# Optimization experiments

Measured on AMD Instinct MI355X. Metric: run time of the kernel, lower is better.

Reference implementation:

```python
import jax, jax.numpy as jnp
import numpy as np

PAD = 0
SOS = 1
NEG = -1e9


def _lstm_scan(x, Wih, Whh, b, h0, c0, reverse=False):
    # x: [T, B, in]; torch gate order i, f, g, o
    def step(carry, xt):
        h, c = carry
        g = xt @ Wih.T + h @ Whh.T + b
        i, f, gg, o = jnp.split(g, 4, axis=-1)
        c = jax.nn.sigmoid(f) * c + jax.nn.sigmoid(i) * jnp.tanh(gg)
        h = jax.nn.sigmoid(o) * jnp.tanh(c)
        return (h, c), h
    (hT, cT), hs = jax.lax.scan(step, (h0, c0), x, reverse=reverse)
    return hs, hT, cT


def setup_inputs() -> dict:
    B, Ts, Tt = 32, 64, 66
    E, H, V = 512, 512, 16000
    key = jax.random.key(0)
    ks = jax.random.split(key, 16)
    s = 0.05
    n = lambda k, shape: (jax.random.normal(k, shape, dtype=jnp.float32) * s)
    return {
        'src_sentences': jax.random.randint(ks[0], (B, Ts), 4, V),
        'trg_sentences': jax.random.randint(ks[1], (B, Tt), 4, V),
        'src_emb': n(ks[2], (V, E)),
        'trg_emb': n(ks[3], (V, E)),
        'enc0_Wih': n(ks[4], (2, 4 * H, E)),
        'enc0_Whh': n(ks[5], (2, 4 * H, H)),
        'enc0_b': n(ks[6], (2, 4 * H)),
        'enc1_Wih': n(ks[7], (2, 4 * H, 2 * H)),
        'enc1_Whh': n(ks[8], (2, 4 * H, H)),
        'enc1_b': n(ks[9], (2, 4 * H)),
        'dec_Wih': n(ks[10], (8 * H, E)),      # LSTMCell: hidden = 2H -> 4*(2H) gates
        'dec_Whh': n(ks[11], (8 * H, 2 * H)),
        'dec_b': n(ks[12], (8 * H)),
        'out_W1': n(ks[13], (H, 4 * H)),
        'out_W2': n(ks[14], (V - 4, H)),
    }


def reference(src_sentences, trg_sentences, src_emb, trg_emb,
              enc0_Wih, enc0_Whh, enc0_b, enc1_Wih, enc1_Whh, enc1_b,
              dec_Wih, dec_Whh, dec_b, out_W1, out_W2):
    B, Ts = src_sentences.shape
    Tt = trg_sentences.shape[1]
    H = out_W1.shape[0]
    dt = src_emb.dtype
    enc_mask = src_sentences == PAD            # [B, Ts] (all False here)

    # ---- encoder: 2-layer bidirectional LSTM (dropout inactive / eval) ----
    x = jnp.swapaxes(src_emb[src_sentences], 0, 1)   # [Ts, B, E]
    z = jnp.zeros((B, H), dt)
    hf0, hfT, cfT = _lstm_scan(x, enc0_Wih[0], enc0_Whh[0], enc0_b[0], z, z)
    hb0, hbT, cbT = _lstm_scan(x, enc0_Wih[1], enc0_Whh[1], enc0_b[1], z, z, reverse=True)
    x1 = jnp.concatenate([hf0, hb0], axis=-1)        # [Ts, B, 2H]
    hf1, _, _ = _lstm_scan(x1, enc1_Wih[0], enc1_Whh[0], enc1_b[0], z, z)
    hb1, _, _ = _lstm_scan(x1, enc1_Wih[1], enc1_Whh[1], enc1_b[1], z, z, reverse=True)
    enc_out = jnp.swapaxes(jnp.concatenate([hf1, hb1], axis=-1), 0, 1)  # [B, Ts, 2H]
    # module uses encoder_hidden_t[0], [1] -> layer-0 fwd/bwd final states
    hidden = jnp.concatenate([hfT, hbT], axis=-1)    # [B, 2H]
    cell = jnp.concatenate([cfT, cbT], axis=-1)

    # ---- decoder: teacher_force = 1.0 (deterministic) ----
    steps = Tt - 2
    emb_in = jnp.swapaxes(trg_emb[trg_sentences[:, :steps]], 0, 1)  # [steps, B, E]
    tgts = jnp.swapaxes(trg_sentences[:, 1:steps + 1], 0, 1)        # [steps, B]

    def step(carry, inp):
        h, c, loss = carry
        xt, tgt = inp
        g = xt @ dec_Wih.T + h @ dec_Whh.T + dec_b
        i, f, gg, o = jnp.split(g, 4, axis=-1)
        c = jax.nn.sigmoid(f) * c + jax.nn.sigmoid(i) * jnp.tanh(gg)
        h = jax.nn.sigmoid(o) * jnp.tanh(c)
        dmask = tgt == PAD
        h = jnp.where(dmask[:, None], jnp.zeros((), dt), h)  # decoder_hidden_t[mask] = 0
        # dot attention over encoder states
        scores = jnp.einsum('btd,bd->bt', enc_out, h)
        scores = jnp.where(enc_mask, NEG, scores)
        attn = jax.nn.softmax(scores, axis=1)
        ctx = jnp.einsum('bt,btd->bd', attn, enc_out)
        zt = jnp.tanh(jnp.concatenate([h, ctx], axis=-1) @ out_W1.T)
        logits = zt @ out_W2.T                                # [B, V-4]
        logp = jax.nn.log_softmax(logits, axis=1)
        tgt_idx = tgt - 4
        valid = tgt_idx != -4                                 # ignore_index=-4 (PAD)
        safe = jnp.where(valid, tgt_idx, 0)
        nll = -jnp.take_along_axis(logp, safe[:, None], axis=1)[:, 0]
        loss = loss + jnp.sum(jnp.where(valid, nll, jnp.zeros((), dt)))
        pred = jnp.argmax(logits, axis=1) + 4
        return (h, c, loss), pred

    (_, _, loss), preds = jax.lax.scan(step, (hidden, cell, jnp.zeros((), dt)), (emb_in, tgts))
    denom = jnp.sum(trg_sentences[:, 1:-1] != PAD).astype(dt)
    return loss / denom, preds.T  # preds: [B, steps]
```

## Files before the change

kernel.cpp:

```cpp
#include <hip/hip_runtime.h>
#include <hip/hip_bf16.h>
#include <math.h>

#define TSRC 64
#define TTRG 66
#define NVOC 15996
#define NTILE 125

__device__ __forceinline__ float sigm(float x){ return 1.f/(1.f+expf(-x)); }

struct GArgs {
  const float* A;  int lda;
  const float* Bw; int ldb;
  const float* bias;
  float* C; int ldc;
  int N; int K; int nNb; int act;
};

template<int BM,int BN,int BK,int TM,int TN>
__global__ __launch_bounds__(256)
void k_gemm(GArgs a)
{
  const int tid = threadIdx.x;
  const int mb = blockIdx.x / a.nNb;
  const int nb = blockIdx.x % a.nNb;
  const int m0 = mb*BM, n0 = nb*BN;
  const float* A  = a.A + (size_t)m0*a.lda;
  const float* Bw = a.Bw;

  __shared__ float As[BK][BM+1];
  __shared__ float Bs[BK][BN+4];
  const int tx = tid % (BN/TN);
  const int ty = tid / (BN/TN);
  float acc[TM][TN];
  #pragma unroll
  for (int i=0;i<TM;i++)
    #pragma unroll
    for (int j=0;j<TN;j++) acc[i][j]=0.f;

  for (int kt=0; kt<a.K; kt+=BK) {
    #pragma unroll
    for (int i=tid; i<BM*BK; i+=256) {
      int m = i/BK, k = i%BK;
      As[k][m] = A[(size_t)m*a.lda + kt + k];
    }
    #pragma unroll
    for (int i=tid; i<BN*BK; i+=256) {
      int n = i/BK, k = i%BK;
      int gn = n0+n;
      Bs[k][n] = (gn < a.N) ? Bw[(size_t)gn*a.ldb + kt + k] : 0.f;
    }
    __syncthreads();
    #pragma unroll
    for (int k=0;k<BK;k++) {
      float av[TM], bv[TN];
      #pragma unroll
      for (int i=0;i<TM;i++) av[i]=As[k][ty*TM+i];
      #pragma unroll
      for (int j=0;j<TN;j++) bv[j]=Bs[k][tx*TN+j];
      #pragma unroll
      for (int i=0;i<TM;i++)
        #pragma unroll
        for (int j=0;j<TN;j++)
          acc[i][j] = fmaf(av[i], bv[j], acc[i][j]);
    }
    __syncthreads();
  }
  #pragma unroll
  for (int i=0;i<TM;i++) {
    int m = m0 + ty*TM + i;
    #pragma unroll
    for (int j=0;j<TN;j++) {
      int n = n0 + tx*TN + j;
      if (n < a.N) {
        float v = acc[i][j];
        if (a.bias) v += a.bias[n];
        if (a.act)  v = tanhf(v);
        a.C[(size_t)m*a.ldc + n] = v;
      }
    }
  }
}

__global__ __launch_bounds__(256)
void k_logits(const float* __restrict__ A, const float* __restrict__ Bw,
              const int* __restrict__ trg,
              float* __restrict__ Pmax, int* __restrict__ Parg,
              float* __restrict__ Psum, float* __restrict__ Ltgt)
{
  const int tid = threadIdx.x;
  const int j8   = blockIdx.x & 7;
  const int mb   = (blockIdx.x >> 3) & 15;
  const int nb   = ((blockIdx.x >> 7) << 3) + j8;
  if (nb >= NTILE) return;
  const int m0 = mb*128, n0 = nb*128;

  __shared__ float As[16][129];
  __shared__ float Bs[16][132];
  const int tx = tid & 15;
  const int ty = tid >> 4;
  float acc[8][8];
  #pragma unroll
  for (int i=0;i<8;i++)
    #pragma unroll
    for (int j=0;j<8;j++) acc[i][j]=0.f;

  for (int kt=0; kt<512; kt+=16) {
    #pragma unroll
    for (int i=tid; i<128*16; i+=256) {
      int m = i>>4, k = i&15;
      As[k][m] = A[(size_t)(m0+m)*512 + kt + k];
    }
    #pragma unroll
    for (int i=tid; i<128*16; i+=256) {
      int n = i>>4, k = i&15;
      int gn = n0+n;
      Bs[k][n] = (gn < NVOC) ? Bw[(size_t)gn*512 + kt + k] : 0.f;
    }
    __syncthreads();
    #pragma unroll
    for (int k=0;k<16;k++) {
      float av[8], bv[8];
      #pragma unroll
      for (int i=0;i<8;i++) av[i]=As[k][ty*8+i];
      #pragma unroll
      for (int j=0;j<8;j++) bv[j]=Bs[k][tx*8+j];
      #pragma unroll
      for (int i=0;i<8;i++)
        #pragma unroll
        for (int j=0;j<8;j++)
          acc[i][j] = fmaf(av[i], bv[j], acc[i][j]);
    }
    __syncthreads();
  }

  #pragma unroll
  for (int i=0;i<8;i++) {
    int r = m0 + ty*8 + i;
    int step = r >> 5, b = r & 31;
    int tgt = trg[b*TTRG + step + 1];
    int ti = tgt - 4;
    float m = -3.4e38f; int am = 0x7fffffff;
    #pragma unroll
    for (int j=0;j<8;j++) {
      int gn = n0 + tx*8 + j;
      if (gn < NVOC) {
        float x = acc[i][j];
        if (x > m || (x == m && gn < am)) { m = x; am = gn; }
      }
    }
    float s = 0.f;
    float lt = 0.f;
    #pragma unroll
    for (int j=0;j<8;j++) {
      int gn = n0 + tx*8 + j;
      if (gn < NVOC) {
        s += expf(acc[i][j] - m);
        if (gn == ti) lt = acc[i][j];
      }
    }
    #pragma unroll
    for (int d=1; d<16; d<<=1) {
      float m2 = __shfl_xor(m, d);
      int   a2 = __shfl_xor(am, d);
      float s2 = __shfl_xor(s, d);
      float l2 = __shfl_xor(lt, d);
      float M = fmaxf(m, m2);
      s = s*expf(m - M) + s2*expf(m2 - M);
      if (m2 > m || (m2 == m && a2 < am)) am = a2;
      m = M;
      lt += l2;
    }
    if (tx == 0) {
      size_t pi = (size_t)r*NTILE + nb;
      Pmax[pi] = m; Parg[pi] = am; Psum[pi] = s;
      if (ti >= n0 && ti < n0 + 128) Ltgt[r] = lt;
    }
  }
}

__global__ __launch_bounds__(128)
void k_combine(const float* __restrict__ Pmax, const int* __restrict__ Parg,
               const float* __restrict__ Psum, const float* __restrict__ Ltgt,
               const int* __restrict__ trg,
               float* __restrict__ nll, float* __restrict__ outp)
{
  int r = blockIdx.x;
  int step = r >> 5, b = r & 31;
  int tid = threadIdx.x;
  __shared__ float sm[128]; __shared__ int sa[128]; __shared__ float ssum[128];
  float m = -3.4e38f; int am = 0x7fffffff; float s = 0.f;
  if (tid < NTILE) {
    size_t pi = (size_t)r*NTILE + tid;
    m = Pmax[pi]; am = Parg[pi]; s = Psum[pi];
  }
  sm[tid]=m; sa[tid]=am; ssum[tid]=s; __syncthreads();
  for (int off=64; off; off>>=1) {
    if (tid < off) {
      float m2 = sm[tid+off]; int a2 = sa[tid+off]; float s2 = ssum[tid+off];
      float m1 = sm[tid];     int a1 = sa[tid];     float s1 = ssum[tid];
      float M = fmaxf(m1, m2);
      ssum[tid] = s1*expf(m1 - M) + s2*expf(m2 - M);
      if (m2 > m1 || (m2 == m1 && a2 < a1)) sa[tid] = a2;
      sm[tid] = M;
    }
    __syncthreads();
  }
  if (tid == 0) {
    int tgt = trg[b*TTRG + step + 1];
    float nl = 0.f;
    if (tgt != 0) nl = -(Ltgt[r] - sm[0] - logf(ssum[0]));
    nll[step*32 + b] = nl;
    outp[1 + b*64 + step] = (float)(sa[0] + 4);
  }
}

__global__ void k_gather(const float* __restrict__ emb, const int* __restrict__ tok,
                         float* __restrict__ outp, int Tfull)
{
  int r = blockIdx.x;
  int t = r >> 5, b = r & 31;
  int token = tok[b*Tfull + t];
  const float4* s = (const float4*)(emb + (size_t)token*512);
  float4* d = (float4*)(outp + (size_t)r*512);
  d[threadIdx.x] = s[threadIdx.x];
}

__global__ __launch_bounds__(256)
void k_rgemm_enc(const float* __restrict__ Whh,
                 const float* __restrict__ hin,
                 float* __restrict__ P)
{
  const int ks  = blockIdx.x >> 5;
  const int rem = blockIdx.x & 31;
  const int dir = rem >> 4;
  const int jt  = rem & 15;
  const int j0  = jt*32;
  const int tid = threadIdx.x;
  const int jcol = tid & 31;
  const int bq   = tid >> 5;
  __shared__ float ws[128][65];
  __shared__ float hs[64][36];
  const float* W = Whh + (size_t)dir*2048*512;
  const float* H = hin + (size_t)dir*32*512;
  float acc[4][4];
  #pragma unroll
  for (int g=0;g<4;g++)
    #pragma unroll
    for (int i=0;i<4;i++) acc[g][i]=0.f;

  for (int kt=ks*128; kt<ks*128+128; kt+=64) {
    for (int idx=tid; idx<128*64; idx+=256) {
      int r = idx >> 6, k = idx & 63;
      int gate = r >> 5, jc = r & 31;
      ws[r][k] = W[(size_t)(gate*512 + j0 + jc)*512 + kt + k];
    }
    for (int idx=tid; idx<32*64; idx+=256) {
      int b = idx >> 6, k = idx & 63;
      hs[k][b] = H[(size_t)b*512 + kt + k];
    }
    __syncthreads();
    #pragma unroll 8
    for (int k=0;k<64;k++) {
      float4 hv = *reinterpret_cast<const float4*>(&hs[k][bq*4]);
      #pragma unroll
      for (int g=0;g<4;g++) {
        float wv = ws[g*32+jcol][k];
        acc[g][0] = fmaf(hv.x, wv, acc[g][0]);
        acc[g][1] = fmaf(hv.y, wv, acc[g][1]);
        acc[g][2] = fmaf(hv.z, wv, acc[g][2]);
        acc[g][3] = fmaf(hv.w, wv, acc[g][3]);
      }
    }
    __syncthreads();
  }
  #pragma unroll
  for (int g=0;g<4;g++)
    #pragma unroll
    for (int i=0;i<4;i++)
      P[((size_t)(ks*2+dir)*32 + bq*4+i)*2048 + g*512 + j0 + jcol] = acc[g][i];
}

__global__ __launch_bounds__(256)
void k_enc_combine(const float* __restrict__ P, const float* __restrict__ xg,
                   float* __restrict__ cst, float* __restrict__ hout,
                   float* __restrict__ xout, int tf, int tb, int mode)
{
  int t = blockIdx.x*256 + threadIdx.x;
  int jh = t & 511, b = (t>>9)&31, dir = t>>14;
  int tt = dir ? tb : tf;
  const float* x = xg + ((size_t)tt*32 + b)*4096 + dir*2048;
  float g4[4];
  #pragma unroll
  for (int g=0; g<4; g++) {
    float s = 0.f;
    #pragma unroll
    for (int ks=0; ks<4; ks++)
      s += P[((size_t)(ks*2+dir)*32 + b)*2048 + g*512 + jh];
    g4[g] = s + x[g*512 + jh];
  }
  size_t ci = ((size_t)dir*32 + b)*512 + jh;
  float cn = sigm(g4[1])*cst[ci] + sigm(g4[0])*tanhf(g4[2]);
  float hn = sigm(g4[3])*tanhf(cn);
  cst[ci] = cn;
  hout[ci] = hn;
  if (mode == 0) xout[((size_t)tt*32 + b)*1024 + dir*512 + jh] = hn;
  else           xout[((size_t)b*64 + tt)*1024 + dir*512 + jh] = hn;
}

__global__ void k_pack(const float* __restrict__ hfin, const float* __restrict__ cfin,
                       float* __restrict__ dh, float* __restrict__ dcc)
{
  int tid = blockIdx.x*256 + threadIdx.x;
  int j = tid & 1023, b = tid >> 10;
  int dir = j >> 9, jj = j & 511;
  size_t si = ((size_t)dir*32 + b)*512 + jj;
  dh[(size_t)b*1024 + j]  = hfin[si];
  dcc[(size_t)b*1024 + j] = cfin[si];
}

__global__ __launch_bounds__(256)
void k_rgemm_dec(const float* __restrict__ Whh,
                 const float* __restrict__ hin,
                 float* __restrict__ P)
{
  const int ks = blockIdx.x >> 5;
  const int jt = blockIdx.x & 31;
  const int j0 = jt*32;
  const int tid = threadIdx.x;
  const int jcol = tid & 31;
  const int bq   = tid >> 5;
  __shared__ float ws[128][65];
  __shared__ float hs[64][36];
  float acc[4][4];
  #pragma unroll
  for (int g=0;g<4;g++)
    #pragma unroll
    for (int i=0;i<4;i++) acc[g][i]=0.f;

  for (int kt=ks*128; kt<ks*128+128; kt+=64) {
    for (int idx=tid; idx<128*64; idx+=256) {
      int r = idx >> 6, k = idx & 63;
      int gate = r >> 5, jc = r & 31;
      ws[r][k] = Whh[(size_t)(gate*1024 + j0 + jc)*1024 + kt + k];
    }
    for (int idx=tid; idx<32*64; idx+=256) {
      int b = idx >> 6, k = idx & 63;
      hs[k][b] = hin[(size_t)b*1024 + kt + k];
    }
    __syncthreads();
    #pragma unroll 8
    for (int k=0;k<64;k++) {
      float4 hv = *reinterpret_cast<const float4*>(&hs[k][bq*4]);
      #pragma unroll
      for (int g=0;g<4;g++) {
        float wv = ws[g*32+jcol][k];
        acc[g][0] = fmaf(hv.x, wv, acc[g][0]);
        acc[g][1] = fmaf(hv.y, wv, acc[g][1]);
        acc[g][2] = fmaf(hv.z, wv, acc[g][2]);
        acc[g][3] = fmaf(hv.w, wv, acc[g][3]);
      }
    }
    __syncthreads();
  }
  #pragma unroll
  for (int g=0;g<4;g++)
    #pragma unroll
    for (int i=0;i<4;i++)
      P[((size_t)ks*32 + bq*4+i)*4096 + g*1024 + j0 + jcol] = acc[g][i];
}

__global__ __launch_bounds__(256)
void k_dec_combine(const float* __restrict__ P, const float* __restrict__ xg_t,
                   float* __restrict__ cst, float* __restrict__ hall_t,
                   const int* __restrict__ trg, int step)
{
  int t = blockIdx.x*256 + threadIdx.x;
  int jh = t & 1023, b = t >> 10;
  int tgt = trg[b*TTRG + step + 1];
  bool dm = (tgt == 0);
  const float* x = xg_t + (size_t)b*4096;
  float g4[4];
  #pragma unroll
  for (int g=0; g<4; g++) {
    float s = 0.f;
    #pragma unroll
    for (int ks=0; ks<8; ks++)
      s += P[((size_t)ks*32 + b)*4096 + g*1024 + jh];
    g4[g] = s + x[g*1024 + jh];
  }
  size_t ci = (size_t)b*1024 + jh;
  float cn = sigm(g4[1])*cst[ci] + sigm(g4[0])*tanhf(g4[2]);
  float hn = sigm(g4[3])*tanhf(cn);
  cst[ci] = cn;
  hall_t[ci] = dm ? 0.f : hn;
}

__global__ __launch_bounds__(256)
void k_attn(const float* __restrict__ Hall,
            const float* __restrict__ encout,
            const int* __restrict__ src,
            float* __restrict__ hctx)
{
  int bid = blockIdx.x;
  int t = bid >> 5, b = bid & 31;
  int tid = threadIdx.x;
  __shared__ float sh[1024];
  __shared__ float ssc[64];
  const float* h = Hall + ((size_t)t*32 + b)*1024;
  size_t row = (size_t)t*32 + b;
  #pragma unroll
  for (int r=0;r<4;r++) {
    int jh = tid + 256*r;
    float v = h[jh];
    sh[jh] = v;
    hctx[row*2048 + jh] = v;
  }
  __syncthreads();
  {
    int tq = tid >> 2, part = tid & 3;
    const float* eo = encout + ((size_t)b*64 + tq)*1024 + part*256;
    const float* hh = sh + part*256;
    float s = 0.f;
    for (int k=0;k<256;k++) s = fmaf(hh[k], eo[k], s);
    s += __shfl_xor(s, 1);
    s += __shfl_xor(s, 2);
    if (part == 0) ssc[tq] = (src[b*TSRC + tq] == 0) ? -1e9f : s;
  }
  __syncthreads();
  if (tid < 64) {
    float v = ssc[tid];
    float m = v;
    for (int d=1; d<64; d<<=1) m = fmaxf(m, __shfl_xor(m, d));
    float e = expf(v - m);
    float su = e;
    for (int d=1; d<64; d<<=1) su += __shfl_xor(su, d);
    ssc[tid] = e / su;
  }
  __syncthreads();
  #pragma unroll
  for (int r=0;r<4;r++) {
    int k = tid + 256*r;
    float a = 0.f;
    const float* eb = encout + (size_t)b*65536 + k;
    for (int tt=0;tt<64;tt++) a = fmaf(ssc[tt], eb[tt*1024], a);
    hctx[row*2048 + 1024 + k] = a;
  }
}

__global__ __launch_bounds__(256)
void k_final(const float* __restrict__ nll, const int* __restrict__ trg,
             float* __restrict__ outp)
{
  int tid = threadIdx.x;
  __shared__ float ss[256]; __shared__ int sc[256];
  float s = 0.f; int cnt = 0;
  for (int i=tid; i<2048; i+=256) {
    s += nll[i];
    int b = i >> 6, t = (i & 63) + 1;
    cnt += (trg[b*TTRG + t] != 0);
  }
  ss[tid]=s; sc[tid]=cnt; __syncthreads();
  for (int off=128; off; off>>=1) {
    if (tid<off) { ss[tid]+=ss[tid+off]; sc[tid]+=sc[tid+off]; }
    __syncthreads();
  }
  if (tid==0) outp[0] = ss[0] / (float)sc[0];
}

static void launch_big(hipStream_t st, const float* A, int lda,
                       const float* Bw, int ldb, const float* bias,
                       float* C, int ldc, int M, int N, int K, int act)
{
  GArgs a;
  a.A=A; a.lda=lda;
  a.Bw=Bw; a.ldb=ldb;
  a.bias=bias;
  a.C=C; a.ldc=ldc;
  a.N=N; a.K=K; a.nNb=(N+127)/128; a.act=act;
  dim3 g((M/128)*a.nNb, 1, 1);
  k_gemm<128,128,16,8,8><<<g, dim3(256), 0, st>>>(a);
}

static void launch_med(hipStream_t st, const float* A, int lda,
                       const float* Bw, int ldb, const float* bias,
                       float* C, int ldc, int M, int N, int K, int act)
{
  GArgs a;
  a.A=A; a.lda=lda;
  a.Bw=Bw; a.ldb=ldb;
  a.bias=bias;
  a.C=C; a.ldc=ldc;
  a.N=N; a.K=K; a.nNb=(N+63)/64; a.act=act;
  dim3 g((M/64)*a.nNb, 1, 1);
  k_gemm<64,64,16,4,4><<<g, dim3(256), 0, st>>>(a);
}

extern "C" void kernel_launch(void* const* d_in, const int* in_sizes, int n_in,
                              void* d_out, int out_size, void* d_ws, size_t ws_size,
                              hipStream_t stream)
{
  (void)in_sizes; (void)n_in; (void)out_size; (void)ws_size;
  const int*   src   = (const int*)  d_in[0];
  const int*   trg   = (const int*)  d_in[1];
  const float* semb  = (const float*)d_in[2];
  const float* temb  = (const float*)d_in[3];
  const float* e0Wih = (const float*)d_in[4];
  const float* e0Whh = (const float*)d_in[5];
  const float* e0b   = (const float*)d_in[6];
  const float* e1Wih = (const float*)d_in[7];
  const float* e1Whh = (const float*)d_in[8];
  const float* e1b   = (const float*)d_in[9];
  const float* dWih  = (const float*)d_in[10];
  const float* dWhh  = (const float*)d_in[11];
  const float* db    = (const float*)d_in[12];
  const float* W1    = (const float*)d_in[13];
  const float* W2    = (const float*)d_in[14];
  float* out = (float*)d_out;

  float* ws = (float*)d_ws;
  size_t o = 0;
  float* x_in   = ws + o; o += (size_t)2048*512;
  float* xg     = ws + o; o += (size_t)2048*4096;
  float* x1     = ws + o; o += (size_t)2048*1024;
  float* encout = ws + o; o += (size_t)2048*1024;
  float* hA     = ws + o; o += 2*32*512;
  float* hB     = ws + o; o += 2*32*512;
  float* cbuf   = ws + o; o += 2*32*512;
  float* dh0    = ws + o; o += 32*1024;
  float* dc     = ws + o; o += 32*1024;
  float* nll    = ws + o; o += 2048;
  float* P      = ws + o; o += (size_t)8*32*4096;
  float* Hall   = x1;
  float* hctx   = xg;
  float* zt     = x_in;
  float* Pmax   = xg + (size_t)4*1024*1024;
  int*   Parg   = (int*)(Pmax + (size_t)2048*NTILE);
  float* Psum   = Pmax + (size_t)2*2048*NTILE;
  float* Ltgt   = Pmax + (size_t)3*2048*NTILE;

  hipMemsetAsync(hA,   0, 2*32*512*sizeof(float), stream);
  hipMemsetAsync(cbuf, 0, 2*32*512*sizeof(float), stream);
  k_gather<<<dim3(2048), dim3(128), 0, stream>>>(semb, src, x_in, TSRC);
  launch_big(stream, x_in, 512, e0Wih, 512, e0b, xg, 4096, 2048, 4096, 512, 0);
  for (int s=0; s<64; s++) {
    float* hin  = (s&1) ? hB : hA;
    float* hout = (s&1) ? hA : hB;
    k_rgemm_enc<<<dim3(128), dim3(256), 0, stream>>>(e0Whh, hin, P);
    k_enc_combine<<<dim3(128), dim3(256), 0, stream>>>(P, xg, cbuf, hout, x1, s, 63-s, 0);
  }
  k_pack<<<dim3(128), dim3(256), 0, stream>>>(hA, cbuf, dh0, dc);

  hipMemsetAsync(hA,   0, 2*32*512*sizeof(float), stream);
  hipMemsetAsync(cbuf, 0, 2*32*512*sizeof(float), stream);
  launch_big(stream, x1, 1024, e1Wih, 1024, e1b, xg, 4096, 2048, 4096, 1024, 0);
  for (int s=0; s<64; s++) {
    float* hin  = (s&1) ? hB : hA;
    float* hout = (s&1) ? hA : hB;
    k_rgemm_enc<<<dim3(128), dim3(256), 0, stream>>>(e1Whh, hin, P);
    k_enc_combine<<<dim3(128), dim3(256), 0, stream>>>(P, xg, cbuf, hout, encout, s, 63-s, 1);
  }

  k_gather<<<dim3(2048), dim3(128), 0, stream>>>(temb, trg, x_in, TTRG);
  launch_big(stream, x_in, 512, dWih, 512, db, xg, 4096, 2048, 4096, 512, 0);
  for (int st=0; st<64; st++) {
    const float* hin = (st == 0) ? dh0 : (Hall + (size_t)(st-1)*32*1024);
    k_rgemm_dec<<<dim3(256), dim3(256), 0, stream>>>(dWhh, hin, P);
    k_dec_combine<<<dim3(128), dim3(256), 0, stream>>>(P, xg + (size_t)st*32*4096,
                 dc, Hall + (size_t)st*32*1024, trg, st);
  }

  k_attn<<<dim3(2048), dim3(256), 0, stream>>>(Hall, encout, src, hctx);
  launch_med(stream, hctx, 2048, W1, 2048, nullptr, zt, 512, 2048, 512, 2048, 1);
  k_logits<<<dim3(2048), dim3(256), 0, stream>>>(zt, W2, trg, Pmax, Parg, Psum, Ltgt);
  k_combine<<<dim3(2048), dim3(128), 0, stream>>>(Pmax, Parg, Psum, Ltgt, trg, nll, out);
  k_final<<<dim3(1), dim3(256), 0, stream>>>(nll, trg, out);
}
```

Measured before the change: 4.628 ms.

## Fuse recurrent GEMM and LSTM cell update into one per-step kernel

Each recurrent timestep now runs a single kernel in place of a split-K GEMM followed by a separate combine kernel. Each block owns 4 hidden units across all four gates and the full K dimension. It keeps h in registers, reduces partial sums through wave shuffles and shared memory, and applies the LSTM cell update directly. This drops the global partial-sum buffer and halves the launches in the 192 sequential steps. In exchange, each block reloads all of h from global memory and does the full-K reduction itself, and register pressure rises from the 16 or 32 float4 values of h held per thread.

Result: faster. 4.261 ms (-7.9%).

```diff
diff --git a/kernel.cpp b/kernel.cpp
--- a/kernel.cpp
+++ b/kernel.cpp
@@ -227,85 +227,163 @@
 }
 
 __global__ __launch_bounds__(256)
-void k_rgemm_enc(const float* __restrict__ Whh,
-                 const float* __restrict__ hin,
-                 float* __restrict__ P)
-{
-  const int ks  = blockIdx.x >> 5;
-  const int rem = blockIdx.x & 31;
-  const int dir = rem >> 4;
-  const int jt  = rem & 15;
-  const int j0  = jt*32;
+void k_estep(const float* __restrict__ Whh,
+             const float* __restrict__ xg,
+             const float* __restrict__ hin,
+             float* __restrict__ hout,
+             float* __restrict__ cst,
+             float* __restrict__ xout, int s, int mode)
+{
+  const int bid = blockIdx.x;
+  const int dir = bid >> 7;
+  const int j0  = (bid & 127) * 4;
   const int tid = threadIdx.x;
-  const int jcol = tid & 31;
-  const int bq   = tid >> 5;
-  __shared__ float ws[128][65];
-  __shared__ float hs[64][36];
-  const float* W = Whh + (size_t)dir*2048*512;
-  const float* H = hin + (size_t)dir*32*512;
-  float acc[4][4];
-  #pragma unroll
-  for (int g=0;g<4;g++)
-    #pragma unroll
-    for (int i=0;i<4;i++) acc[g][i]=0.f;
-
-  for (int kt=ks*128; kt<ks*128+128; kt+=64) {
-    for (int idx=tid; idx<128*64; idx+=256) {
-      int r = idx >> 6, k = idx & 63;
-      int gate = r >> 5, jc = r & 31;
-      ws[r][k] = W[(size_t)(gate*512 + j0 + jc)*512 + kt + k];
-    }
-    for (int idx=tid; idx<32*64; idx+=256) {
-      int b = idx >> 6, k = idx & 63;
-      hs[k][b] = H[(size_t)b*512 + kt + k];
-    }
-    __syncthreads();
-    #pragma unroll 8
-    for (int k=0;k<64;k++) {
-      float4 hv = *reinterpret_cast<const float4*>(&hs[k][bq*4]);
-      #pragma unroll
-      for (int g=0;g<4;g++) {
-        float wv = ws[g*32+jcol][k];
-        acc[g][0] = fmaf(hv.x, wv, acc[g][0]);
-        acc[g][1] = fmaf(hv.y, wv, acc[g][1]);
-        acc[g][2] = fmaf(hv.z, wv, acc[g][2]);
-        acc[g][3] = fmaf(hv.w, wv, acc[g][3]);
+  const int kg  = tid >> 5;
+  const int b   = tid & 31;
+  __shared__ float4 wl4[16*128];
+  __shared__ float red[4*16*33];
+
+  {
+    const float* W = Whh + (size_t)dir*2048*512;
+    for (int idx = tid; idx < 16*128; idx += 256) {
+      int r = idx >> 7, c = idx & 127;
+      int g = r >> 2, jj = r & 3;
+      wl4[idx] = ((const float4*)(W + (size_t)(g*512 + j0 + jj)*512))[c];
+    }
+  }
+  float4 hreg[16];
+  {
+    const float4* H4 = (const float4*)(hin + (size_t)dir*32*512);
+    #pragma unroll
+    for (int j=0;j<16;j++) hreg[j] = H4[(size_t)b*128 + kg*16 + j];
+  }
+  __syncthreads();
+
+  float acc[16];
+  #pragma unroll
+  for (int r=0;r<16;r++) {
+    const float4* wr = wl4 + r*128 + kg*16;
+    float a0=0.f,a1=0.f,a2=0.f,a3=0.f;
+    #pragma unroll
+    for (int j=0;j<16;j++) {
+      float4 w = wr[j];
+      a0 = fmaf(w.x, hreg[j].x, a0);
+      a1 = fmaf(w.y, hreg[j].y, a1);
+      a2 = fmaf(w.z, hreg[j].z, a2);
+      a3 = fmaf(w.w, hreg[j].w, a3);
+    }
+    acc[r] = (a0+a1)+(a2+a3);
+  }
+  #pragma unroll
+  for (int r=0;r<16;r++) acc[r] += __shfl_xor(acc[r], 32);
+  const int wv = tid >> 6;
+  if ((tid & 32) == 0) {
+    #pragma unroll
+    for (int r=0;r<16;r++) red[wv*528 + r*33 + b] = acc[r];
+  }
+  __syncthreads();
+
+  if (tid < 128) {
+    int jj = tid >> 5, bb = tid & 31;
+    int jh = j0 + jj;
+    int t  = dir ? (63 - s) : s;
+    const float* x = xg + ((size_t)t*32 + bb)*4096 + dir*2048;
+    float g4[4];
+    #pragma unroll
+    for (int g=0; g<4; g++) {
+      int r = g*4 + jj;
+      g4[g] = ((red[0*528 + r*33 + bb] + red[1*528 + r*33 + bb])
+             + (red[2*528 + r*33 + bb] + red[3*528 + r*33 + bb]))
+             + x[g*512 + jh];
+    }
+    size_t ci = ((size_t)dir*32 + bb)*512 + jh;
+    float cn = sigm(g4[1])*cst[ci] + sigm(g4[0])*tanhf(g4[2]);
+    float hn = sigm(g4[3])*tanhf(cn);
+    cst[ci] = cn;
+    hout[ci] = hn;
+    if (mode == 0) xout[((size_t)t*32 + bb)*1024 + dir*512 + jh] = hn;
+    else           xout[((size_t)bb*64 + t)*1024 + dir*512 + jh] = hn;
+  }
+}
+
+__global__ __launch_bounds__(256)
+void k_dstep(const float* __restrict__ Whh,
+             const float* __restrict__ xg_t,
+             const float* __restrict__ hin,
+             float* __restrict__ cst,
+             float* __restrict__ hall_t,
+             const int* __restrict__ trg, int st)
+{
+  const int bid = blockIdx.x;
+  const int j0  = bid*4;
+  const int tid = threadIdx.x;
+  const int kg  = tid >> 5;
+  const int b   = tid & 31;
+  __shared__ float4 wl4[8*256];
+  __shared__ float red[4*16*33];
+
+  float4 hreg[32];
+  {
+    const float4* H4 = (const float4*)hin;
+    #pragma unroll
+    for (int j=0;j<32;j++) hreg[j] = H4[(size_t)b*256 + kg*32 + j];
+  }
+
+  float acc[16];
+  #pragma unroll
+  for (int hh=0; hh<2; hh++) {
+    for (int idx = tid; idx < 8*256; idx += 256) {
+      int rl = idx >> 8, c = idx & 255;
+      int r = hh*8 + rl;
+      int g = r >> 2, jj = r & 3;
+      wl4[idx] = ((const float4*)(Whh + (size_t)(g*1024 + j0 + jj)*1024))[c];
+    }
+    __syncthreads();
+    #pragma unroll
+    for (int rl=0; rl<8; rl++) {
+      const float4* wr = wl4 + rl*256 + kg*32;
+      float a0=0.f,a1=0.f,a2=0.f,a3=0.f;
+      #pragma unroll
+      for (int j=0;j<32;j++) {
+        float4 w = wr[j];
+        a0 = fmaf(w.x, hreg[j].x, a0);
+        a1 = fmaf(w.y, hreg[j].y, a1);
+        a2 = fmaf(w.z, hreg[j].z, a2);
+        a3 = fmaf(w.w, hreg[j].w, a3);
       }
-    }
-    __syncthreads();
-  }
-  #pragma unroll
-  for (int g=0;g<4;g++)
-    #pragma unroll
-    for (int i=0;i<4;i++)
-      P[((size_t)(ks*2+dir)*32 + bq*4+i)*2048 + g*512 + j0 + jcol] = acc[g][i];
-}
-
-__global__ __launch_bounds__(256)
-void k_enc_combine(const float* __restrict__ P, const float* __restrict__ xg,
-                   float* __restrict__ cst, float* __restrict__ hout,
-                   float* __restrict__ xout, int tf, int tb, int mode)
-{
-  int t = blockIdx.x*256 + threadIdx.x;
-  int jh = t & 511, b = (t>>9)&31, dir = t>>14;
-  int tt = dir ? tb : tf;
-  const float* x = xg + ((size_t)tt*32 + b)*4096 + dir*2048;
-  float g4[4];
-  #pragma unroll
-  for (int g=0; g<4; g++) {
-    float s = 0.f;
-    #pragma unroll
-    for (int ks=0; ks<4; ks++)
-      s += P[((size_t)(ks*2+dir)*32 + b)*2048 + g*512 + jh];
-    g4[g] = s + x[g*512 + jh];
-  }
-  size_t ci = ((size_t)dir*32 + b)*512 + jh;
-  float cn = sigm(g4[1])*cst[ci] + sigm(g4[0])*tanhf(g4[2]);
-  float hn = sigm(g4[3])*tanhf(cn);
-  cst[ci] = cn;
-  hout[ci] = hn;
-  if (mode == 0) xout[((size_t)tt*32 + b)*1024 + dir*512 + jh] = hn;
-  else           xout[((size_t)b*64 + tt)*1024 + dir*512 + jh] = hn;
+      acc[hh*8 + rl] = (a0+a1)+(a2+a3);
+    }
+    __syncthreads();
+  }
+  #pragma unroll
+  for (int r=0;r<16;r++) acc[r] += __shfl_xor(acc[r], 32);
+  const int wv = tid >> 6;
+  if ((tid & 32) == 0) {
+    #pragma unroll
+    for (int r=0;r<16;r++) red[wv*528 + r*33 + b] = acc[r];
+  }
+  __syncthreads();
+
+  if (tid < 128) {
+    int jj = tid >> 5, bb = tid & 31;
+    int jh = j0 + jj;
+    int tgt = trg[bb*TTRG + st + 1];
+    bool dm = (tgt == 0);
+    const float* x = xg_t + (size_t)bb*4096;
+    float g4[4];
+    #pragma unroll
+    for (int g=0; g<4; g++) {
+      int r = g*4 + jj;
+      g4[g] = ((red[0*528 + r*33 + bb] + red[1*528 + r*33 + bb])
+             + (red[2*528 + r*33 + bb] + red[3*528 + r*33 + bb]))
+             + x[g*1024 + jh];
+    }
+    size_t ci = (size_t)bb*1024 + jh;
+    float cn = sigm(g4[1])*cst[ci] + sigm(g4[0])*tanhf(g4[2]);
+    float hn = sigm(g4[3])*tanhf(cn);
+    cst[ci] = cn;
+    hall_t[ci] = dm ? 0.f : hn;
+  }
 }
 
 __global__ void k_pack(const float* __restrict__ hfin, const float* __restrict__ cfin,
@@ -317,83 +395,6 @@
   size_t si = ((size_t)dir*32 + b)*512 + jj;
   dh[(size_t)b*1024 + j]  = hfin[si];
   dcc[(size_t)b*1024 + j] = cfin[si];
-}
-
-__global__ __launch_bounds__(256)
-void k_rgemm_dec(const float* __restrict__ Whh,
-                 const float* __restrict__ hin,
-                 float* __restrict__ P)
-{
-  const int ks = blockIdx.x >> 5;
-  const int jt = blockIdx.x & 31;
-  const int j0 = jt*32;
-  const int tid = threadIdx.x;
-  const int jcol = tid & 31;
-  const int bq   = tid >> 5;
-  __shared__ float ws[128][65];
-  __shared__ float hs[64][36];
-  float acc[4][4];
-  #pragma unroll
-  for (int g=0;g<4;g++)
-    #pragma unroll
-    for (int i=0;i<4;i++) acc[g][i]=0.f;
-
-  for (int kt=ks*128; kt<ks*128+128; kt+=64) {
-    for (int idx=tid; idx<128*64; idx+=256) {
-      int r = idx >> 6, k = idx & 63;
-      int gate = r >> 5, jc = r & 31;
-      ws[r][k] = Whh[(size_t)(gate*1024 + j0 + jc)*1024 + kt + k];
-    }
-    for (int idx=tid; idx<32*64; idx+=256) {
-      int b = idx >> 6, k = idx & 63;
-      hs[k][b] = hin[(size_t)b*1024 + kt + k];
-    }
-    __syncthreads();
-    #pragma unroll 8
-    for (int k=0;k<64;k++) {
-      float4 hv = *reinterpret_cast<const float4*>(&hs[k][bq*4]);
-      #pragma unroll
-      for (int g=0;g<4;g++) {
-        float wv = ws[g*32+jcol][k];
-        acc[g][0] = fmaf(hv.x, wv, acc[g][0]);
-        acc[g][1] = fmaf(hv.y, wv, acc[g][1]);
-        acc[g][2] = fmaf(hv.z, wv, acc[g][2]);
-        acc[g][3] = fmaf(hv.w, wv, acc[g][3]);
-      }
-    }
-    __syncthreads();
-  }
-  #pragma unroll
-  for (int g=0;g<4;g++)
-    #pragma unroll
-    for (int i=0;i<4;i++)
-      P[((size_t)ks*32 + bq*4+i)*4096 + g*1024 + j0 + jcol] = acc[g][i];
-}
-
-__global__ __launch_bounds__(256)
-void k_dec_combine(const float* __restrict__ P, const float* __restrict__ xg_t,
-                   float* __restrict__ cst, float* __restrict__ hall_t,
-                   const int* __restrict__ trg, int step)
-{
-  int t = blockIdx.x*256 + threadIdx.x;
-  int jh = t & 1023, b = t >> 10;
-  int tgt = trg[b*TTRG + step + 1];
-  bool dm = (tgt == 0);
-  const float* x = xg_t + (size_t)b*4096;
-  float g4[4];
-  #pragma unroll
-  for (int g=0; g<4; g++) {
-    float s = 0.f;
-    #pragma unroll
-    for (int ks=0; ks<8; ks++)
-      s += P[((size_t)ks*32 + b)*4096 + g*1024 + jh];
-    g4[g] = s + x[g*1024 + jh];
-  }
-  size_t ci = (size_t)b*1024 + jh;
-  float cn = sigm(g4[1])*cst[ci] + sigm(g4[0])*tanhf(g4[2]);
-  float hn = sigm(g4[3])*tanhf(cn);
-  cst[ci] = cn;
-  hall_t[ci] = dm ? 0.f : hn;
 }
 
 __global__ __launch_bounds__(256)
@@ -530,7 +531,6 @@
   float* dh0    = ws + o; o += 32*1024;
   float* dc     = ws + o; o += 32*1024;
   float* nll    = ws + o; o += 2048;
-  float* P      = ws + o; o += (size_t)8*32*4096;
   float* Hall   = x1;
   float* hctx   = xg;
   float* zt     = x_in;
@@ -546,8 +546,7 @@
   for (int s=0; s<64; s++) {
     float* hin  = (s&1) ? hB : hA;
     float* hout = (s&1) ? hA : hB;
-    k_rgemm_enc<<<dim3(128), dim3(256), 0, stream>>>(e0Whh, hin, P);
-    k_enc_combine<<<dim3(128), dim3(256), 0, stream>>>(P, xg, cbuf, hout, x1, s, 63-s, 0);
+    k_estep<<<dim3(256), dim3(256), 0, stream>>>(e0Whh, xg, hin, hout, cbuf, x1, s, 0);
   }
   k_pack<<<dim3(128), dim3(256), 0, stream>>>(hA, cbuf, dh0, dc);
 
@@ -557,17 +556,15 @@
   for (int s=0; s<64; s++) {
     float* hin  = (s&1) ? hB : hA;
     float* hout = (s&1) ? hA : hB;
-    k_rgemm_enc<<<dim3(128), dim3(256), 0, stream>>>(e1Whh, hin, P);
-    k_enc_combine<<<dim3(128), dim3(256), 0, stream>>>(P, xg, cbuf, hout, encout, s, 63-s, 1);
+    k_estep<<<dim3(256), dim3(256), 0, stream>>>(e1Whh, xg, hin, hout, cbuf, encout, s, 1);
   }
 
   k_gather<<<dim3(2048), dim3(128), 0, stream>>>(temb, trg, x_in, TTRG);
   launch_big(stream, x_in, 512, dWih, 512, db, xg, 4096, 2048, 4096, 512, 0);
   for (int st=0; st<64; st++) {
     const float* hin = (st == 0) ? dh0 : (Hall + (size_t)(st-1)*32*1024);
-    k_rgemm_dec<<<dim3(256), dim3(256), 0, stream>>>(dWhh, hin, P);
-    k_dec_combine<<<dim3(128), dim3(256), 0, stream>>>(P, xg + (size_t)st*32*4096,
-                 dc, Hall + (size_t)st*32*1024, trg, st);
+    k_dstep<<<dim3(256), dim3(256), 0, stream>>>(dWhh, xg + (size_t)st*32*4096,
+                 hin, dc, Hall + (size_t)st*32*1024, trg, st);
   }
 
   k_attn<<<dim3(2048), dim3(256), 0, stream>>>(Hall, encout, src, hctx);
```
